# Optimization experiments

Hardware: AMD Instinct MI355X
Metric: run time of the kernel (lower is better)

Reference implementation:

```python
import jax, jax.numpy as jnp
import numpy as np

T = 8          # time steps (init kwarg T)
GAMA = 1.0     # ZIF surrogate width (init kwarg gama)
LR = 0.1       # adaptive-threshold learning rate (init kwarg learning_rate)
THRESH = 8.0   # init kwarg thresh

# ZIF spiking activation: heaviside forward, triangular surrogate backward
@jax.custom_vjp
def heaviside(u):
    return (u >= 0).astype(u.dtype)

def _hv_fwd(u):
    return (u >= 0).astype(u.dtype), u

def _hv_bwd(u, g):
    surr = (1.0 / GAMA) * (1.0 / GAMA) * jnp.maximum(GAMA - jnp.abs(u), 0.0)
    return (g * surr,)

heaviside.defvjp(_hv_fwd, _hv_bwd)


def setup_inputs() -> dict:
    key = jax.random.key(0)
    x = jax.random.normal(key, (T * 32, 128, 32, 32), dtype=jnp.float32)  # [T*B, C, H, W]
    thresh = jnp.full((1,), THRESH, dtype=jnp.float32)                    # learnable thresh param
    return {"x": x, "thresh": thresh}


def reference(x, thresh):
    # thresh is used via .data in torch -> detached
    thre = jax.lax.stop_gradient(thresh)[0]
    B = x.shape[0] // T
    xs = x.reshape((T, B) + x.shape[1:])           # [T, B, C, H, W]
    C = xs.shape[2]
    neuron_thre0 = jnp.full((C,), thre, x.dtype)   # per-channel threshold init
    cur = neuron_thre0.reshape(1, C, 1, 1)         # broadcasts over [B, C, H, W]

    # sequential IF recurrence over T, carrying membrane potential
    def step(mem, xt):
        mem = mem + xt
        s = heaviside(mem - cur)
        mem = mem - s * cur
        return mem, s

    mem0 = jnp.broadcast_to(0.5 * cur, xs.shape[1:]).astype(x.dtype)
    mem, spikes = jax.lax.scan(step, mem0, xs)     # spikes: [T, B, C, H, W]

    # compensation pass over the stacked spike history
    compen_mem = mem - 0.5 * cur
    spike_count = spikes.sum(axis=0)               # [B, C, H, W]
    compen_value = jnp.minimum(compen_mem + spike_count * cur, T * cur)
    pos = (compen_value > 0) & (spike_count > 0)
    safe_count = jnp.where(spike_count > 0, spike_count, jnp.ones_like(spike_count))
    new_thre = jnp.where(pos, compen_value / safe_count, jnp.zeros_like(compen_value))

    # adaptive threshold update (scalar gradient-descent style step)
    ub = new_thre.mean(axis=(0, 2, 3))             # [C] per-channel target
    diff = ub - neuron_thre0
    mask = jax.lax.stop_gradient((neuron_thre0 > ub).astype(x.dtype))
    update = LR * 2.0 * (diff * mask).mean()       # scalar
    neuron_thre = neuron_thre0 + update            # [C]

    # scale spikes by the updated per-channel threshold, merge temporal dim
    out = spikes * neuron_thre.reshape(1, 1, C, 1, 1)
    return out.reshape((T * B,) + x.shape[1:])
```

## Files before the change

kernel.cpp:

```cpp
#include <hip/hip_runtime.h>
#include <stdint.h>

static constexpr int   T_  = 8;
static constexpr int   C_  = 128;
static constexpr int   N_  = 32 * 128 * 32 * 32;
static constexpr int   NBLK_ = N_ / 4 / 256;
static constexpr float LR_ = 0.1f;

typedef float v4f __attribute__((ext_vector_type(4)));

template <bool PACK>
__global__ __launch_bounds__(256) void k_fwd(const float* __restrict__ x,
                                             const float* __restrict__ thresh,
                                             uint8_t* __restrict__ spk,
                                             float* __restrict__ part) {
    const float thre = thresh[0];
    const int e4   = blockIdx.x * 256 + threadIdx.x;
    const int base = e4 * 4;

    float    mem[4];
    int      cnt[4] = {0, 0, 0, 0};
    unsigned pb[4]  = {0, 0, 0, 0};
#pragma unroll
    for (int i = 0; i < 4; ++i) mem[i] = 0.5f * thre;

#pragma unroll
    for (int t = 0; t < T_; ++t) {
        const v4f xv = __builtin_nontemporal_load(
            reinterpret_cast<const v4f*>(x + (size_t)t * N_ + base));
#pragma unroll
        for (int i = 0; i < 4; ++i) {
            mem[i] += xv[i];
            if (mem[i] - thre >= 0.0f) {
                mem[i] -= thre;
                pb[i] |= (1u << t);
                cnt[i]++;
            }
        }
    }

    if (PACK) {
        const unsigned packed = pb[0] | (pb[1] << 8) | (pb[2] << 16) | (pb[3] << 24);
        reinterpret_cast<unsigned*>(spk)[e4] = packed;
    }

    float local = 0.0f;
#pragma unroll
    for (int i = 0; i < 4; ++i) {
        const float compen_mem = mem[i] - 0.5f * thre;
        const float cv = fminf(compen_mem + (float)cnt[i] * thre, (float)T_ * thre);
        if (cv > 0.0f && cnt[i] > 0) local += cv / (float)cnt[i];
    }

#pragma unroll
    for (int off = 32; off > 0; off >>= 1) local += __shfl_down(local, off, 64);
    __shared__ float wpart[4];
    const int lane = threadIdx.x & 63;
    const int wid  = threadIdx.x >> 6;
    if (lane == 0) wpart[wid] = local;
    __syncthreads();
    if (threadIdx.x == 0) {
        part[blockIdx.x] = wpart[0] + wpart[1] + wpart[2] + wpart[3];
    }
}

__device__ __forceinline__ float compute_scalar(const float* __restrict__ part,
                                                const float thre,
                                                float* s_red) {
    float v = 0.0f;
    if (threadIdx.x < C_) {
        float sum = 0.0f;
#pragma unroll
        for (int g = 0; g < NBLK_ / C_; ++g) sum += part[g * C_ + threadIdx.x];
        const float ub = sum * (1.0f / 32768.0f);
        v = (thre > ub) ? (ub - thre) : 0.0f;
    }
#pragma unroll
    for (int off = 32; off > 0; off >>= 1) v += __shfl_down(v, off, 64);
    if ((threadIdx.x & 63) == 0) s_red[1 + (threadIdx.x >> 6)] = v;
    __syncthreads();
    if (threadIdx.x == 0) {
        const float update =
            LR_ * 2.0f * (s_red[1] + s_red[2] + s_red[3] + s_red[4]) * (1.0f / (float)C_);
        s_red[0] = thre + update;
    }
    __syncthreads();
    return s_red[0];
}

__global__ __launch_bounds__(256) void k_out(const uint8_t* __restrict__ spk,
                                             const float* __restrict__ part,
                                             const float* __restrict__ thresh,
                                             float* __restrict__ out) {
    __shared__ float s_red[5];
    const float s = compute_scalar(part, thresh[0], s_red);

    const int e4   = blockIdx.x * 256 + threadIdx.x;
    const int base = e4 * 4;
    const unsigned packed = reinterpret_cast<const unsigned*>(spk)[e4];
    const unsigned pb[4] = {packed & 0xffu, (packed >> 8) & 0xffu,
                            (packed >> 16) & 0xffu, (packed >> 24) & 0xffu};
#pragma unroll
    for (int t = 0; t < T_; ++t) {
        v4f o;
        o.x = ((pb[0] >> t) & 1) ? s : 0.0f;
        o.y = ((pb[1] >> t) & 1) ? s : 0.0f;
        o.z = ((pb[2] >> t) & 1) ? s : 0.0f;
        o.w = ((pb[3] >> t) & 1) ? s : 0.0f;
        __builtin_nontemporal_store(o, reinterpret_cast<v4f*>(out + (size_t)t * N_ + base));
    }
}

__global__ __launch_bounds__(256) void k_out_recompute(const float* __restrict__ x,
                                                       const float* __restrict__ part,
                                                       const float* __restrict__ thresh,
                                                       float* __restrict__ out) {
    __shared__ float s_red[5];
    const float thre = thresh[0];
    const float s = compute_scalar(part, thre, s_red);

    const int e4   = blockIdx.x * 256 + threadIdx.x;
    const int base = e4 * 4;
    float mem[4];
#pragma unroll
    for (int i = 0; i < 4; ++i) mem[i] = 0.5f * thre;
#pragma unroll
    for (int t = 0; t < T_; ++t) {
        const v4f xv = __builtin_nontemporal_load(
            reinterpret_cast<const v4f*>(x + (size_t)t * N_ + base));
        v4f o;
#pragma unroll
        for (int i = 0; i < 4; ++i) {
            mem[i] += xv[i];
            if (mem[i] - thre >= 0.0f) {
                mem[i] -= thre;
                o[i] = s;
            } else {
                o[i] = 0.0f;
            }
        }
        __builtin_nontemporal_store(o, reinterpret_cast<v4f*>(out + (size_t)t * N_ + base));
    }
}

extern "C" void kernel_launch(void* const* d_in, const int* in_sizes, int n_in,
                              void* d_out, int out_size, void* d_ws, size_t ws_size,
                              hipStream_t stream) {
    const float* x      = (const float*)d_in[0];
    const float* thresh = (const float*)d_in[1];
    float*       out    = (float*)d_out;

    float*   part = (float*)d_ws;
    uint8_t* spk  = (uint8_t*)d_ws + NBLK_ * sizeof(float);
    const bool pack = ws_size >= (size_t)(NBLK_ * sizeof(float) + N_);

    if (pack) {
        k_fwd<true><<<NBLK_, 256, 0, stream>>>(x, thresh, spk, part);
        k_out<<<NBLK_, 256, 0, stream>>>(spk, part, thresh, out);
    } else {
        k_fwd<false><<<NBLK_, 256, 0, stream>>>(x, thresh, nullptr, part);
        k_out_recompute<<<NBLK_, 256, 0, stream>>>(x, part, thresh, out);
    }
}
```

Measured before the change: 55.94 us.

## Fuse forward and output passes into one cooperative kernel with grid sync

Replaces the two-kernel pipeline with a single cooperative kernel of 1024 blocks. Each thread handles four chunks, keeps the packed spike bits in registers, and a grid-wide sync separates the per-block partial sums from the output write. This removes the spike-bit round trip through global workspace and the second kernel launch. In exchange it adds a grid barrier and needs all 1024 blocks to be co-resident, and it falls back to the old path if the cooperative launch fails.

```diff
diff --git a/kernel.cpp b/kernel.cpp
--- a/kernel.cpp
+++ b/kernel.cpp
@@ -1,13 +1,101 @@
 #include <hip/hip_runtime.h>
+#include <hip/hip_cooperative_groups.h>
 #include <stdint.h>
 
-static constexpr int   T_  = 8;
-static constexpr int   C_  = 128;
-static constexpr int   N_  = 32 * 128 * 32 * 32;
-static constexpr int   NBLK_ = N_ / 4 / 256;
-static constexpr float LR_ = 0.1f;
+namespace cg = cooperative_groups;
+
+static constexpr int   T_     = 8;
+static constexpr int   C_     = 128;
+static constexpr int   N_     = 32 * 128 * 32 * 32;
+static constexpr int   CHUNK_ = N_ / 4;
+static constexpr int   NBLKC_ = 1024;
+static constexpr int   NBLK_  = N_ / 4 / 256;
+static constexpr float LR_    = 0.1f;
 
 typedef float v4f __attribute__((ext_vector_type(4)));
+
+__global__ __launch_bounds__(256, 4) void k_fused(const float* __restrict__ x,
+                                                  const float* __restrict__ thresh,
+                                                  float* __restrict__ part,
+                                                  float* __restrict__ out) {
+    const float thre = thresh[0];
+    const int tid = threadIdx.x;
+    const int b   = blockIdx.x;
+
+    unsigned pbp[4];
+    float local = 0.0f;
+
+#pragma unroll
+    for (int k = 0; k < 4; ++k) {
+        const size_t base = (size_t)k * CHUNK_ + (size_t)b * 1024 + tid * 4;
+        float    mem[4];
+        unsigned pb[4] = {0, 0, 0, 0};
+#pragma unroll
+        for (int i = 0; i < 4; ++i) mem[i] = 0.5f * thre;
+#pragma unroll
+        for (int t = 0; t < T_; ++t) {
+            const v4f xv = __builtin_nontemporal_load(
+                reinterpret_cast<const v4f*>(x + (size_t)t * N_ + base));
+#pragma unroll
+            for (int i = 0; i < 4; ++i) {
+                mem[i] += xv[i];
+                if (mem[i] - thre >= 0.0f) {
+                    mem[i] -= thre;
+                    pb[i] |= (1u << t);
+                }
+            }
+        }
+        pbp[k] = pb[0] | (pb[1] << 8) | (pb[2] << 16) | (pb[3] << 24);
+#pragma unroll
+        for (int i = 0; i < 4; ++i) {
+            const int   cnt = __popc(pb[i]);
+            const float compen_mem = mem[i] - 0.5f * thre;
+            const float cv = fminf(compen_mem + (float)cnt * thre, (float)T_ * thre);
+            if (cv > 0.0f && cnt > 0) local += cv / (float)cnt;
+        }
+    }
+
+#pragma unroll
+    for (int off = 32; off > 0; off >>= 1) local += __shfl_down(local, off, 64);
+    __shared__ float sm[8];
+    const int lane = tid & 63;
+    const int wid  = tid >> 6;
+    if (lane == 0) sm[wid] = local;
+    __syncthreads();
+    if (tid == 0) part[b] = sm[0] + sm[1] + sm[2] + sm[3];
+
+    cg::this_grid().sync();
+
+    float v = 0.0f;
+    if (tid < C_) {
+        float sum = 0.0f;
+#pragma unroll
+        for (int g = 0; g < NBLKC_ / C_; ++g) sum += part[g * C_ + tid];
+        const float ub = sum * (1.0f / 32768.0f);
+        v = (thre > ub) ? (ub - thre) : 0.0f;
+    }
+#pragma unroll
+    for (int off = 32; off > 0; off >>= 1) v += __shfl_down(v, off, 64);
+    __syncthreads();
+    if (lane == 0) sm[4 + wid] = v;
+    __syncthreads();
+    const float s = thre + LR_ * 2.0f * (sm[4] + sm[5] + sm[6] + sm[7]) * (1.0f / (float)C_);
+
+#pragma unroll
+    for (int k = 0; k < 4; ++k) {
+        const size_t base = (size_t)k * CHUNK_ + (size_t)b * 1024 + tid * 4;
+        const unsigned pk = pbp[k];
+#pragma unroll
+        for (int t = 0; t < T_; ++t) {
+            v4f o;
+            o.x = ((pk >> t) & 1)        ? s : 0.0f;
+            o.y = ((pk >> (8 + t)) & 1)  ? s : 0.0f;
+            o.z = ((pk >> (16 + t)) & 1) ? s : 0.0f;
+            o.w = ((pk >> (24 + t)) & 1) ? s : 0.0f;
+            __builtin_nontemporal_store(o, reinterpret_cast<v4f*>(out + (size_t)t * N_ + base));
+        }
+    }
+}
 
 template <bool PACK>
 __global__ __launch_bounds__(256) void k_fwd(const float* __restrict__ x,
@@ -17,13 +105,10 @@
     const float thre = thresh[0];
     const int e4   = blockIdx.x * 256 + threadIdx.x;
     const int base = e4 * 4;
-
     float    mem[4];
-    int      cnt[4] = {0, 0, 0, 0};
-    unsigned pb[4]  = {0, 0, 0, 0};
+    unsigned pb[4] = {0, 0, 0, 0};
 #pragma unroll
     for (int i = 0; i < 4; ++i) mem[i] = 0.5f * thre;
-
 #pragma unroll
     for (int t = 0; t < T_; ++t) {
         const v4f xv = __builtin_nontemporal_load(
@@ -31,27 +116,21 @@
 #pragma unroll
         for (int i = 0; i < 4; ++i) {
             mem[i] += xv[i];
-            if (mem[i] - thre >= 0.0f) {
-                mem[i] -= thre;
-                pb[i] |= (1u << t);
-                cnt[i]++;
-            }
-        }
-    }
-
+            if (mem[i] - thre >= 0.0f) { mem[i] -= thre; pb[i] |= (1u << t); }
+        }
+    }
     if (PACK) {
-        const unsigned packed = pb[0] | (pb[1] << 8) | (pb[2] << 16) | (pb[3] << 24);
-        reinterpret_cast<unsigned*>(spk)[e4] = packed;
-    }
-
+        reinterpret_cast<unsigned*>(spk)[e4] =
+            pb[0] | (pb[1] << 8) | (pb[2] << 16) | (pb[3] << 24);
+    }
     float local = 0.0f;
 #pragma unroll
     for (int i = 0; i < 4; ++i) {
+        const int   cnt = __popc(pb[i]);
         const float compen_mem = mem[i] - 0.5f * thre;
-        const float cv = fminf(compen_mem + (float)cnt[i] * thre, (float)T_ * thre);
-        if (cv > 0.0f && cnt[i] > 0) local += cv / (float)cnt[i];
-    }
-
+        const float cv = fminf(compen_mem + (float)cnt * thre, (float)T_ * thre);
+        if (cv > 0.0f && cnt > 0) local += cv / (float)cnt;
+    }
 #pragma unroll
     for (int off = 32; off > 0; off >>= 1) local += __shfl_down(local, off, 64);
     __shared__ float wpart[4];
@@ -59,14 +138,11 @@
     const int wid  = threadIdx.x >> 6;
     if (lane == 0) wpart[wid] = local;
     __syncthreads();
-    if (threadIdx.x == 0) {
-        part[blockIdx.x] = wpart[0] + wpart[1] + wpart[2] + wpart[3];
-    }
-}
-
-__device__ __forceinline__ float compute_scalar(const float* __restrict__ part,
-                                                const float thre,
-                                                float* s_red) {
+    if (threadIdx.x == 0) part[blockIdx.x] = wpart[0] + wpart[1] + wpart[2] + wpart[3];
+}
+
+__device__ __forceinline__ float compute_scalar4k(const float* __restrict__ part,
+                                                  const float thre, float* s_red) {
     float v = 0.0f;
     if (threadIdx.x < C_) {
         float sum = 0.0f;
@@ -80,9 +156,8 @@
     if ((threadIdx.x & 63) == 0) s_red[1 + (threadIdx.x >> 6)] = v;
     __syncthreads();
     if (threadIdx.x == 0) {
-        const float update =
-            LR_ * 2.0f * (s_red[1] + s_red[2] + s_red[3] + s_red[4]) * (1.0f / (float)C_);
-        s_red[0] = thre + update;
+        s_red[0] = thre + LR_ * 2.0f *
+                   (s_red[1] + s_red[2] + s_red[3] + s_red[4]) * (1.0f / (float)C_);
     }
     __syncthreads();
     return s_red[0];
@@ -93,20 +168,17 @@
                                              const float* __restrict__ thresh,
                                              float* __restrict__ out) {
     __shared__ float s_red[5];
-    const float s = compute_scalar(part, thresh[0], s_red);
-
+    const float s = compute_scalar4k(part, thresh[0], s_red);
     const int e4   = blockIdx.x * 256 + threadIdx.x;
     const int base = e4 * 4;
     const unsigned packed = reinterpret_cast<const unsigned*>(spk)[e4];
-    const unsigned pb[4] = {packed & 0xffu, (packed >> 8) & 0xffu,
-                            (packed >> 16) & 0xffu, (packed >> 24) & 0xffu};
 #pragma unroll
     for (int t = 0; t < T_; ++t) {
         v4f o;
-        o.x = ((pb[0] >> t) & 1) ? s : 0.0f;
-        o.y = ((pb[1] >> t) & 1) ? s : 0.0f;
-        o.z = ((pb[2] >> t) & 1) ? s : 0.0f;
-        o.w = ((pb[3] >> t) & 1) ? s : 0.0f;
+        o.x = ((packed >> t) & 1)        ? s : 0.0f;
+        o.y = ((packed >> (8 + t)) & 1)  ? s : 0.0f;
+        o.z = ((packed >> (16 + t)) & 1) ? s : 0.0f;
+        o.w = ((packed >> (24 + t)) & 1) ? s : 0.0f;
         __builtin_nontemporal_store(o, reinterpret_cast<v4f*>(out + (size_t)t * N_ + base));
     }
 }
@@ -117,8 +189,7 @@
                                                        float* __restrict__ out) {
     __shared__ float s_red[5];
     const float thre = thresh[0];
-    const float s = compute_scalar(part, thre, s_red);
-
+    const float s = compute_scalar4k(part, thre, s_red);
     const int e4   = blockIdx.x * 256 + threadIdx.x;
     const int base = e4 * 4;
     float mem[4];
@@ -132,12 +203,8 @@
 #pragma unroll
         for (int i = 0; i < 4; ++i) {
             mem[i] += xv[i];
-            if (mem[i] - thre >= 0.0f) {
-                mem[i] -= thre;
-                o[i] = s;
-            } else {
-                o[i] = 0.0f;
-            }
+            if (mem[i] - thre >= 0.0f) { mem[i] -= thre; o[i] = s; }
+            else                        { o[i] = 0.0f; }
         }
         __builtin_nontemporal_store(o, reinterpret_cast<v4f*>(out + (size_t)t * N_ + base));
     }
@@ -152,8 +219,14 @@
 
     float*   part = (float*)d_ws;
     uint8_t* spk  = (uint8_t*)d_ws + NBLK_ * sizeof(float);
+
+    void* args[] = {(void*)&x, (void*)&thresh, (void*)&part, (void*)&out};
+    hipError_t e = hipLaunchCooperativeKernel((const void*)k_fused, dim3(NBLKC_),
+                                              dim3(256), args, 0, stream);
+    if (e == hipSuccess) return;
+    (void)hipGetLastError();
+
     const bool pack = ws_size >= (size_t)(NBLK_ * sizeof(float) + N_);
-
     if (pack) {
         k_fwd<true><<<NBLK_, 256, 0, stream>>>(x, thresh, spk, part);
         k_out<<<NBLK_, 256, 0, stream>>>(spk, part, thresh, out);
```

Result: slower. 156.8 us (+180.2%).

## Split scalar reduction into its own kernel and remap output fill per time step

Applied to the files above, without the earlier changes.

The per-block recomputation of the threshold scalar (each output block re-reading all partial sums) moves into a single tiny kernel that writes the scalar to workspace. The output kernel is remapped so each block handles one time step and a contiguous 16K-site slab, giving each block one contiguous write stream. The forward kernel also drops the spike counter in favour of popcount, switches x loads from nontemporal to normal, and stores the packed spikes nontemporally. The cost is one extra kernel launch, and the spike bytes are now read eight times instead of once.

```diff
diff --git a/kernel.cpp b/kernel.cpp
--- a/kernel.cpp
+++ b/kernel.cpp
@@ -1,11 +1,12 @@
 #include <hip/hip_runtime.h>
 #include <stdint.h>
 
-static constexpr int   T_  = 8;
-static constexpr int   C_  = 128;
-static constexpr int   N_  = 32 * 128 * 32 * 32;
+static constexpr int   T_    = 8;
+static constexpr int   C_    = 128;
+static constexpr int   N_    = 32 * 128 * 32 * 32;
+static constexpr int   N4_   = N_ / 4;
 static constexpr int   NBLK_ = N_ / 4 / 256;
-static constexpr float LR_ = 0.1f;
+static constexpr float LR_   = 0.1f;
 
 typedef float v4f __attribute__((ext_vector_type(4)));
 
@@ -17,41 +18,35 @@
     const float thre = thresh[0];
     const int e4   = blockIdx.x * 256 + threadIdx.x;
     const int base = e4 * 4;
-
     float    mem[4];
-    int      cnt[4] = {0, 0, 0, 0};
-    unsigned pb[4]  = {0, 0, 0, 0};
+    unsigned pb[4] = {0, 0, 0, 0};
 #pragma unroll
     for (int i = 0; i < 4; ++i) mem[i] = 0.5f * thre;
-
 #pragma unroll
     for (int t = 0; t < T_; ++t) {
-        const v4f xv = __builtin_nontemporal_load(
-            reinterpret_cast<const v4f*>(x + (size_t)t * N_ + base));
+        const v4f xv = *reinterpret_cast<const v4f*>(x + (size_t)t * N_ + base);
 #pragma unroll
         for (int i = 0; i < 4; ++i) {
             mem[i] += xv[i];
             if (mem[i] - thre >= 0.0f) {
                 mem[i] -= thre;
                 pb[i] |= (1u << t);
-                cnt[i]++;
             }
         }
     }
-
     if (PACK) {
-        const unsigned packed = pb[0] | (pb[1] << 8) | (pb[2] << 16) | (pb[3] << 24);
-        reinterpret_cast<unsigned*>(spk)[e4] = packed;
+        __builtin_nontemporal_store(
+            pb[0] | (pb[1] << 8) | (pb[2] << 16) | (pb[3] << 24),
+            reinterpret_cast<unsigned*>(spk) + e4);
     }
-
     float local = 0.0f;
 #pragma unroll
     for (int i = 0; i < 4; ++i) {
+        const int   cnt = __popc(pb[i]);
         const float compen_mem = mem[i] - 0.5f * thre;
-        const float cv = fminf(compen_mem + (float)cnt[i] * thre, (float)T_ * thre);
-        if (cv > 0.0f && cnt[i] > 0) local += cv / (float)cnt[i];
+        const float cv = fminf(compen_mem + (float)cnt * thre, (float)T_ * thre);
+        if (cv > 0.0f && cnt > 0) local += cv / (float)cnt;
     }
-
 #pragma unroll
     for (int off = 32; off > 0; off >>= 1) local += __shfl_down(local, off, 64);
     __shared__ float wpart[4];
@@ -59,66 +54,55 @@
     const int wid  = threadIdx.x >> 6;
     if (lane == 0) wpart[wid] = local;
     __syncthreads();
+    if (threadIdx.x == 0) part[blockIdx.x] = wpart[0] + wpart[1] + wpart[2] + wpart[3];
+}
+
+__global__ __launch_bounds__(128) void k_scalar(const float* __restrict__ part,
+                                                const float* __restrict__ thresh,
+                                                float* __restrict__ scal) {
+    const float thre = thresh[0];
+    float sum = 0.0f;
+#pragma unroll
+    for (int g = 0; g < NBLK_ / C_; ++g) sum += part[g * C_ + threadIdx.x];
+    const float ub = sum * (1.0f / 32768.0f);
+    float v = (thre > ub) ? (ub - thre) : 0.0f;
+#pragma unroll
+    for (int off = 32; off > 0; off >>= 1) v += __shfl_down(v, off, 64);
+    __shared__ float partial[2];
+    if ((threadIdx.x & 63) == 0) partial[threadIdx.x >> 6] = v;
+    __syncthreads();
     if (threadIdx.x == 0) {
-        part[blockIdx.x] = wpart[0] + wpart[1] + wpart[2] + wpart[3];
+        scal[0] = thre + LR_ * 2.0f * (partial[0] + partial[1]) * (1.0f / (float)C_);
     }
 }
 
-__device__ __forceinline__ float compute_scalar(const float* __restrict__ part,
-                                                const float thre,
-                                                float* s_red) {
-    float v = 0.0f;
-    if (threadIdx.x < C_) {
-        float sum = 0.0f;
+__global__ __launch_bounds__(256) void k_out_fill(const uint8_t* __restrict__ spk,
+                                                  const float* __restrict__ scal,
+                                                  float* __restrict__ out) {
+    const float s = scal[0];
+    const int t = blockIdx.x >> 8;
+    const int site4_base = (blockIdx.x & 255) * 4096;
+    const unsigned* sp32 = reinterpret_cast<const unsigned*>(spk);
 #pragma unroll
-        for (int g = 0; g < NBLK_ / C_; ++g) sum += part[g * C_ + threadIdx.x];
-        const float ub = sum * (1.0f / 32768.0f);
-        v = (thre > ub) ? (ub - thre) : 0.0f;
-    }
-#pragma unroll
-    for (int off = 32; off > 0; off >>= 1) v += __shfl_down(v, off, 64);
-    if ((threadIdx.x & 63) == 0) s_red[1 + (threadIdx.x >> 6)] = v;
-    __syncthreads();
-    if (threadIdx.x == 0) {
-        const float update =
-            LR_ * 2.0f * (s_red[1] + s_red[2] + s_red[3] + s_red[4]) * (1.0f / (float)C_);
-        s_red[0] = thre + update;
-    }
-    __syncthreads();
-    return s_red[0];
-}
-
-__global__ __launch_bounds__(256) void k_out(const uint8_t* __restrict__ spk,
-                                             const float* __restrict__ part,
-                                             const float* __restrict__ thresh,
-                                             float* __restrict__ out) {
-    __shared__ float s_red[5];
-    const float s = compute_scalar(part, thresh[0], s_red);
-
-    const int e4   = blockIdx.x * 256 + threadIdx.x;
-    const int base = e4 * 4;
-    const unsigned packed = reinterpret_cast<const unsigned*>(spk)[e4];
-    const unsigned pb[4] = {packed & 0xffu, (packed >> 8) & 0xffu,
-                            (packed >> 16) & 0xffu, (packed >> 24) & 0xffu};
-#pragma unroll
-    for (int t = 0; t < T_; ++t) {
+    for (int it = 0; it < 16; ++it) {
+        const int i4 = it * 256 + threadIdx.x;
+        const unsigned p = sp32[site4_base + i4];
         v4f o;
-        o.x = ((pb[0] >> t) & 1) ? s : 0.0f;
-        o.y = ((pb[1] >> t) & 1) ? s : 0.0f;
-        o.z = ((pb[2] >> t) & 1) ? s : 0.0f;
-        o.w = ((pb[3] >> t) & 1) ? s : 0.0f;
-        __builtin_nontemporal_store(o, reinterpret_cast<v4f*>(out + (size_t)t * N_ + base));
+        o.x = ((p >> t) & 1)        ? s : 0.0f;
+        o.y = ((p >> (8 + t)) & 1)  ? s : 0.0f;
+        o.z = ((p >> (16 + t)) & 1) ? s : 0.0f;
+        o.w = ((p >> (24 + t)) & 1) ? s : 0.0f;
+        __builtin_nontemporal_store(
+            o, reinterpret_cast<v4f*>(out) + (size_t)t * N4_ + site4_base + i4);
     }
 }
 
 __global__ __launch_bounds__(256) void k_out_recompute(const float* __restrict__ x,
-                                                       const float* __restrict__ part,
                                                        const float* __restrict__ thresh,
+                                                       const float* __restrict__ scal,
                                                        float* __restrict__ out) {
-    __shared__ float s_red[5];
     const float thre = thresh[0];
-    const float s = compute_scalar(part, thre, s_red);
-
+    const float s    = scal[0];
     const int e4   = blockIdx.x * 256 + threadIdx.x;
     const int base = e4 * 4;
     float mem[4];
@@ -126,18 +110,13 @@
     for (int i = 0; i < 4; ++i) mem[i] = 0.5f * thre;
 #pragma unroll
     for (int t = 0; t < T_; ++t) {
-        const v4f xv = __builtin_nontemporal_load(
-            reinterpret_cast<const v4f*>(x + (size_t)t * N_ + base));
+        const v4f xv = *reinterpret_cast<const v4f*>(x + (size_t)t * N_ + base);
         v4f o;
 #pragma unroll
         for (int i = 0; i < 4; ++i) {
             mem[i] += xv[i];
-            if (mem[i] - thre >= 0.0f) {
-                mem[i] -= thre;
-                o[i] = s;
-            } else {
-                o[i] = 0.0f;
-            }
+            if (mem[i] - thre >= 0.0f) { mem[i] -= thre; o[i] = s; }
+            else                        { o[i] = 0.0f; }
         }
         __builtin_nontemporal_store(o, reinterpret_cast<v4f*>(out + (size_t)t * N_ + base));
     }
@@ -151,14 +130,17 @@
     float*       out    = (float*)d_out;
 
     float*   part = (float*)d_ws;
-    uint8_t* spk  = (uint8_t*)d_ws + NBLK_ * sizeof(float);
-    const bool pack = ws_size >= (size_t)(NBLK_ * sizeof(float) + N_);
+    float*   scal = (float*)((uint8_t*)d_ws + 16384);
+    uint8_t* spk  = (uint8_t*)d_ws + 32768;
+    const bool pack = ws_size >= (size_t)(32768 + N_);
 
     if (pack) {
         k_fwd<true><<<NBLK_, 256, 0, stream>>>(x, thresh, spk, part);
-        k_out<<<NBLK_, 256, 0, stream>>>(spk, part, thresh, out);
+        k_scalar<<<1, 128, 0, stream>>>(part, thresh, scal);
+        k_out_fill<<<T_ * 256, 256, 0, stream>>>(spk, scal, out);
     } else {
         k_fwd<false><<<NBLK_, 256, 0, stream>>>(x, thresh, nullptr, part);
-        k_out_recompute<<<NBLK_, 256, 0, stream>>>(x, part, thresh, out);
+        k_scalar<<<1, 128, 0, stream>>>(part, thresh, scal);
+        k_out_recompute<<<NBLK_, 256, 0, stream>>>(x, thresh, scal, out);
     }
 }
```

Result: no change. 54.89 us (-1.9%).
